# Kernel tuning notes

Measured on AMD Instinct MI355X. Metric: run time of the kernel, lower is better.

The kernel has to match this reference:

```python
import jax, jax.numpy as jnp
import numpy as np

TAU = 2.0        # LIF membrane time constant
VTH = 1.0        # spike threshold
VRESET = 0.0     # hard reset voltage
ALPHA = 2.0      # ATan surrogate alpha
LN_EPS = 1e-5


@jax.custom_vjp
def atan_spike(x):
    # Heaviside forward, ATan surrogate backward (spikingjelly surrogate.ATan)
    return (x >= 0.0).astype(x.dtype)

def _atan_fwd(x):
    return atan_spike(x), x

def _atan_bwd(x, g):
    z = (jnp.pi / 2.0) * ALPHA * x
    return (g * (ALPHA / 2.0) / (1.0 + z * z),)

atan_spike.defvjp(_atan_fwd, _atan_bwd)


def layer_norm(x, w, b):
    mu = jnp.mean(x, axis=-1, keepdims=True)
    var = jnp.mean(jnp.square(x - mu), axis=-1, keepdims=True)
    return (x - mu) * jax.lax.rsqrt(var + LN_EPS) * w + b


def time_shift(x):
    # x: [B,T,C] -> x shifted by one step in time, zero-padded at t=0
    return jnp.pad(x, ((0, 0), (1, 0), (0, 0)))[:, :-1]


def wkv(time_decay, time_first, k, v):
    # Numerically-stable RWKV WKV recurrence. k, v: [B,T,C]
    w = -jnp.exp(time_decay)  # [C]
    u = time_first            # [C]
    B, T, C = k.shape
    kT = jnp.moveaxis(k, 1, 0)  # [T,B,C]
    vT = jnp.moveaxis(v, 1, 0)
    init = (jnp.zeros((B, C), k.dtype),
            jnp.zeros((B, C), k.dtype),
            jnp.full((B, C), -1e38, k.dtype))

    def step(carry, kv_t):
        aa, bb, pp = carry
        kt, vt = kv_t
        ww = u + kt
        p = jnp.maximum(pp, ww)
        e1 = jnp.exp(pp - p)
        e2 = jnp.exp(ww - p)
        y = (e1 * aa + e2 * vt) / (e1 * bb + e2)
        ww2 = pp + w
        p2 = jnp.maximum(ww2, kt)
        e1b = jnp.exp(ww2 - p2)
        e2b = jnp.exp(kt - p2)
        return (e1b * aa + e2b * vt, e1b * bb + e2b, p2), y

    _, yT = jax.lax.scan(step, init, (kT, vT))
    return jnp.moveaxis(yT, 0, 1)  # [B,T,C]


def lif(x):
    # MultiStepLIFNode: tau=2, decay_input=True, v_th=1, hard reset to 0.
    # Recurrence runs over the sequence dim (permute(1,0,2) in torch is layout only).
    xT = jnp.moveaxis(x, 1, 0)  # [T,B,C]
    v0 = jnp.zeros_like(xT[0])

    def step(v, xt):
        v = v + (xt - (v - VRESET)) / TAU
        s = atan_spike(v - VTH)
        v = (1.0 - s) * v + s * VRESET
        return v, s

    _, sT = jax.lax.scan(step, v0, xT)
    return jnp.moveaxis(sT, 0, 1)


def rwkv_time_mix(x, time_decay, time_first, mix_k, mix_v, mix_r, Wk, Wv, Wr, Wo):
    xx = time_shift(x)
    xk = x * mix_k + xx * (1.0 - mix_k)
    xv = x * mix_v + xx * (1.0 - mix_v)
    xr = x * mix_r + xx * (1.0 - mix_r)
    k = jnp.einsum('btc,cd->btd', xk, Wk)
    v = jnp.einsum('btc,cd->btd', xv, Wv)
    r = jax.nn.sigmoid(jnp.einsum('btc,cd->btd', xr, Wr))
    y = wkv(time_decay, time_first, k, v)
    return jnp.einsum('btc,cd->btd', r * y, Wo)


def rwkv_channel_mix(x, mix_k, mix_r, Wk, Wv, Wr):
    xx = time_shift(x)
    xk = x * mix_k + xx * (1.0 - mix_k)
    xr = x * mix_r + xx * (1.0 - mix_r)
    k = jnp.square(jax.nn.relu(jnp.einsum('btc,ch->bth', xk, Wk)))  # relu^2
    kv = jnp.einsum('bth,hc->btc', k, Wv)
    return jax.nn.sigmoid(jnp.einsum('btc,cd->btd', xr, Wr)) * kv


def setup_inputs() -> dict:
    key = jax.random.key(0)
    B, T, C, H = 8, 2048, 768, 3072
    ks = jax.random.split(key, 20)
    p = lambda k, shape, s=0.02: (jax.random.normal(k, shape, jnp.float32) * s)
    u = lambda k, shape: jax.random.uniform(k, shape, jnp.float32)
    return {
        'x': jax.random.normal(ks[0], (B, T, C), jnp.float32),
        'ln1_w': jnp.ones((C,), jnp.float32), 'ln1_b': jnp.zeros((C,), jnp.float32),
        'ln2_w': jnp.ones((C,), jnp.float32), 'ln2_b': jnp.zeros((C,), jnp.float32),
        'att_time_decay': p(ks[1], (C,), 1.0),
        'att_time_first': p(ks[2], (C,), 1.0),
        'att_mix_k': u(ks[3], (C,)), 'att_mix_v': u(ks[4], (C,)), 'att_mix_r': u(ks[5], (C,)),
        'att_Wk': p(ks[6], (C, C)), 'att_Wv': p(ks[7], (C, C)),
        'att_Wr': p(ks[8], (C, C)), 'att_Wo': p(ks[9], (C, C)),
        'ffn_mix_k': u(ks[10], (C,)), 'ffn_mix_r': u(ks[11], (C,)),
        'ffn_Wk': p(ks[12], (C, H)), 'ffn_Wv': p(ks[13], (H, C)), 'ffn_Wr': p(ks[14], (C, C)),
    }


def reference(x, ln1_w, ln1_b, ln2_w, ln2_b,
              att_time_decay, att_time_first, att_mix_k, att_mix_v, att_mix_r,
              att_Wk, att_Wv, att_Wr, att_Wo,
              ffn_mix_k, ffn_mix_r, ffn_Wk, ffn_Wv, ffn_Wr):
    # Block.forward with layer_id != 0 (no ln0, att path); dropout in eval mode.
    a = rwkv_time_mix(layer_norm(x, ln1_w, ln1_b), att_time_decay, att_time_first,
                      att_mix_k, att_mix_v, att_mix_r, att_Wk, att_Wv, att_Wr, att_Wo)
    x = x + lif(a)
    f = rwkv_channel_mix(layer_norm(x, ln2_w, ln2_b), ffn_mix_k, ffn_mix_r,
                         ffn_Wk, ffn_Wv, ffn_Wr)
    x = x + lif(f)
    return x
```

## Files before the change

kernel.cpp:

```cpp
#include <hip/hip_runtime.h>

#define B_ 8
#define T_ 2048
#define C_ 768
#define H_ 3072
#define BT_ (B_ * T_)
#define BC_ (B_ * C_)
#define WSEG 128
#define NWSEG 16
#define LSEG 128
#define NLSEG 16
#define LWARM 96

typedef unsigned short u16;
typedef short bf16x8 __attribute__((ext_vector_type(8)));
typedef float f32x4 __attribute__((ext_vector_type(4)));

__device__ __forceinline__ float b2f(u16 u) {
    union { unsigned i; float f; } w; w.i = ((unsigned)u) << 16; return w.f;
}
__device__ __forceinline__ u16 f2b(float f) {
    union { float f; unsigned i; } w; w.f = f;
    return (u16)((w.i + 0x7fffu + ((w.i >> 16) & 1u)) >> 16);
}

typedef __attribute__((address_space(3))) unsigned int lds_u32;
typedef const __attribute__((address_space(1))) unsigned int glb_u32;
__device__ __forceinline__ void gld_lds16(const void* g, void* l) {
    __builtin_amdgcn_global_load_lds((glb_u32*)g, (lds_u32*)l, 16, 0, 0);
}

template<int NOUT>
__global__ void lnmix(const float* __restrict__ x, const float* __restrict__ w,
                      const float* __restrict__ b,
                      const float* __restrict__ m1, const float* __restrict__ m2,
                      const float* __restrict__ m3,
                      u16* __restrict__ o1, u16* __restrict__ o2, u16* __restrict__ o3) {
    int row = blockIdx.x;
    int t = row % T_;
    const float* xr = x + (size_t)row * C_;
    const float* xp = xr - C_;
    int tid = threadIdx.x;
    float s = 0.f, s2 = 0.f, ps = 0.f, ps2 = 0.f;
    for (int i = tid; i < C_; i += 256) {
        float v = xr[i]; s += v; s2 += v * v;
        if (t > 0) { float u = xp[i]; ps += u; ps2 += u * u; }
    }
    for (int off = 32; off > 0; off >>= 1) {
        s += __shfl_down(s, off);  s2 += __shfl_down(s2, off);
        ps += __shfl_down(ps, off); ps2 += __shfl_down(ps2, off);
    }
    __shared__ float red[4][4];
    int wid = tid >> 6, lane = tid & 63;
    if (lane == 0) { red[wid][0] = s; red[wid][1] = s2; red[wid][2] = ps; red[wid][3] = ps2; }
    __syncthreads();
    if (tid == 0) {
        float a0 = 0, a1 = 0, a2 = 0, a3 = 0;
        for (int i = 0; i < 4; ++i) { a0 += red[i][0]; a1 += red[i][1]; a2 += red[i][2]; a3 += red[i][3]; }
        red[0][0] = a0; red[0][1] = a1; red[0][2] = a2; red[0][3] = a3;
    }
    __syncthreads();
    float mu = red[0][0] * (1.f / C_);
    float rs = rsqrtf(red[0][1] * (1.f / C_) - mu * mu + 1e-5f);
    float pmu = red[0][2] * (1.f / C_);
    float prs = rsqrtf(red[0][3] * (1.f / C_) - pmu * pmu + 1e-5f);
    size_t ob = (size_t)row * C_;
    for (int i = tid; i < C_; i += 256) {
        float wi = w[i], bi = b[i];
        float n = (xr[i] - mu) * rs * wi + bi;
        float np = (t > 0) ? (xp[i] - pmu) * prs * wi + bi : 0.f;
        o1[ob + i] = f2b(fmaf(m1[i], n - np, np));
        o2[ob + i] = f2b(fmaf(m2[i], n - np, np));
        if constexpr (NOUT == 3) o3[ob + i] = f2b(fmaf(m3[i], n - np, np));
    }
}

struct TCJ { const float* s; u16* d; int R, Ncol, nbx, b0; };
struct TC7 { TCJ j[7]; };
__global__ void tcast_all(TC7 jobs) {
    __shared__ float t[32][33];
    int bid = blockIdx.x;
    int ji = 0;
#pragma unroll
    for (int k = 1; k < 7; ++k) if (bid >= jobs.j[k].b0) ji = k;
    TCJ jb = jobs.j[ji];
    int local = bid - jb.b0;
    int bx = local % jb.nbx, by = local / jb.nbx;
    int c0 = bx * 32, r0 = by * 32;
    int col = threadIdx.x & 31, rw = threadIdx.x >> 5;
#pragma unroll
    for (int i = 0; i < 4; ++i) {
        int r = rw + i * 8;
        t[r][col] = jb.s[(size_t)(r0 + r) * jb.Ncol + c0 + col];
    }
    __syncthreads();
#pragma unroll
    for (int i = 0; i < 4; ++i) {
        int r = rw + i * 8;
        jb.d[(size_t)(c0 + r) * jb.R + r0 + col] = f2b(t[col][r]);
    }
}

__device__ __forceinline__ void gemm_core(const u16* __restrict__ A,
                                          const u16* __restrict__ WT,
                                          int K, int m0, int n0,
                                          u16* As, u16* Bs, f32x4 acc[4][8]) {
    const int tid = threadIdx.x;
    const int lane = tid & 63, wid = tid >> 6;
    const int wr = wid >> 1, wc = wid & 1;
    const int r16 = lane & 15, g = lane >> 4;

    const int srow = tid >> 2;
    const int sslot = tid & 3;
    const int sx = (srow >> 1) & 3;
    const u16* gA0 = A + (size_t)(m0 + srow) * K + ((sslot ^ sx) << 3);
    const u16* gA1 = gA0 + (size_t)64 * K;
    const u16* gB0 = WT + (size_t)(n0 + srow) * K + ((sslot ^ sx) << 3);
    const u16* gB1 = gB0 + (size_t)64 * K;
    const u16* gB2 = gB0 + (size_t)128 * K;
    const u16* gB3 = gB0 + (size_t)192 * K;
    u16* lA = As + tid * 8;
    u16* lB = Bs + tid * 8;

    int offA[4], offB[8];
#pragma unroll
    for (int m = 0; m < 4; ++m) {
        int row = wr * 64 + m * 16 + r16;
        offA[m] = row * 32 + (g ^ ((row >> 1) & 3)) * 8;
    }
#pragma unroll
    for (int n = 0; n < 8; ++n) {
        int rob = wc * 128 + n * 16 + r16;
        offB[n] = rob * 32 + (g ^ ((rob >> 1) & 3)) * 8;
    }

    gld_lds16(gA0, lA);        gld_lds16(gA1, lA + 2048);
    gld_lds16(gB0, lB);        gld_lds16(gB1, lB + 2048);
    gld_lds16(gB2, lB + 4096); gld_lds16(gB3, lB + 6144);
    gA0 += 32; gA1 += 32; gB0 += 32; gB1 += 32; gB2 += 32; gB3 += 32;
    __syncthreads();

    const int nk = K >> 5;
    int cur = 0;
    for (int kt = 0; kt < nk; ++kt) {
        const int nxt = cur ^ 1;
        if (kt + 1 < nk) {
            u16* pA = lA + nxt * 4096;
            u16* pB = lB + nxt * 8192;
            gld_lds16(gA0, pA);        gld_lds16(gA1, pA + 2048);
            gld_lds16(gB0, pB);        gld_lds16(gB1, pB + 2048);
            gld_lds16(gB2, pB + 4096); gld_lds16(gB3, pB + 6144);
            gA0 += 32; gA1 += 32; gB0 += 32; gB1 += 32; gB2 += 32; gB3 += 32;
        }
        const u16* Ab = As + cur * 4096;
        const u16* Bb = Bs + cur * 8192;
        bf16x8 af[4], bg[8];
#pragma unroll
        for (int m = 0; m < 4; ++m) af[m] = *(const bf16x8*)(Ab + offA[m]);
#pragma unroll
        for (int n = 0; n < 8; ++n) bg[n] = *(const bf16x8*)(Bb + offB[n]);
#pragma unroll
        for (int m = 0; m < 4; ++m)
#pragma unroll
            for (int n = 0; n < 8; ++n)
                acc[m][n] = __builtin_amdgcn_mfma_f32_16x16x32_bf16(af[m], bg[n], acc[m][n], 0, 0, 0);
        __syncthreads();
        cur = nxt;
    }
}

__device__ __forceinline__ void xcd_remap(int& m0, int& n0) {
    const int gx = gridDim.x;
    const int nwg = gx * gridDim.y;
    const int lin = blockIdx.y * gx + blockIdx.x;
    const int q = nwg >> 3, r = nwg & 7;
    const int xcd = lin & 7, pos = lin >> 3;
    const int nid = (xcd < r ? xcd * (q + 1) : r * (q + 1) + (xcd - r) * q) + pos;
    m0 = (nid / gx) << 7;
    n0 = (nid % gx) << 8;
}

template<int MODE, bool EMUL>
__global__ __launch_bounds__(256, 2)
void gemm2(const u16* __restrict__ A, const u16* __restrict__ WT,
           u16* __restrict__ Cout, const u16* __restrict__ Emul, int N, int K) {
    __shared__ u16 As[8192];
    __shared__ u16 Bs[16384];
    int m0, n0;
    xcd_remap(m0, n0);
    f32x4 acc[4][8];
#pragma unroll
    for (int i = 0; i < 4; ++i)
#pragma unroll
        for (int j = 0; j < 8; ++j)
#pragma unroll
            for (int q = 0; q < 4; ++q) acc[i][j][q] = 0.f;
    gemm_core(A, WT, K, m0, n0, As, Bs, acc);

    const int lane = threadIdx.x & 63, wid = threadIdx.x >> 6;
    const int wr = wid >> 1, wc = wid & 1;
    const int r16 = lane & 15, g = lane >> 4;
#pragma unroll
    for (int m = 0; m < 4; ++m)
#pragma unroll
        for (int n = 0; n < 8; ++n)
#pragma unroll
            for (int j = 0; j < 4; ++j) {
                int row = m0 + wr * 64 + m * 16 + g * 4 + j;
                int col = n0 + wc * 128 + n * 16 + r16;
                float v = acc[m][n][j];
                if constexpr (MODE == 1) v = 1.f / (1.f + expf(-v));
                if constexpr (MODE == 2) { v = fmaxf(v, 0.f); v = v * v; }
                size_t o = (size_t)row * N + col;
                if constexpr (EMUL) v *= b2f(Emul[o]);
                Cout[o] = f2b(v);
            }
}

struct P3 {
    const u16 *A0, *A1, *A2;
    const u16 *W0, *W1, *W2;
    u16 *O0, *O1, *O2;
};
__global__ __launch_bounds__(256, 2)
void proj3(P3 p, int N, int K) {
    __shared__ u16 As[8192];
    __shared__ u16 Bs[16384];
    const int z = blockIdx.z;
    const u16* A = (z == 0) ? p.A0 : (z == 1) ? p.A1 : p.A2;
    const u16* W = (z == 0) ? p.W0 : (z == 1) ? p.W1 : p.W2;
    u16* O = (z == 0) ? p.O0 : (z == 1) ? p.O1 : p.O2;
    int m0, n0;
    xcd_remap(m0, n0);
    f32x4 acc[4][8];
#pragma unroll
    for (int i = 0; i < 4; ++i)
#pragma unroll
        for (int j = 0; j < 8; ++j)
#pragma unroll
            for (int q = 0; q < 4; ++q) acc[i][j][q] = 0.f;
    gemm_core(A, W, K, m0, n0, As, Bs, acc);

    const int lane = threadIdx.x & 63, wid = threadIdx.x >> 6;
    const int wr = wid >> 1, wc = wid & 1;
    const int r16 = lane & 15, g = lane >> 4;
    const bool sig = (z == 2);
#pragma unroll
    for (int m = 0; m < 4; ++m)
#pragma unroll
        for (int n = 0; n < 8; ++n)
#pragma unroll
            for (int j = 0; j < 4; ++j) {
                int row = m0 + wr * 64 + m * 16 + g * 4 + j;
                int col = n0 + wc * 128 + n * 16 + r16;
                float v = acc[m][n][j];
                if (sig) v = 1.f / (1.f + expf(-v));
                O[(size_t)row * N + col] = f2b(v);
            }
}

__global__ void wkv_p1(const float* __restrict__ td, const u16* __restrict__ K,
                       const u16* __restrict__ V, float* __restrict__ st) {
    int bc = blockIdx.x * 256 + threadIdx.x;
    int seg = blockIdx.y;
    int b = bc / C_, c = bc - b * C_;
    float w = -expf(td[c]);
    size_t off = (size_t)b * T_ * C_ + (size_t)seg * WSEG * C_ + c;
    float aa = 0.f, bb = 0.f, pp = -1e38f;
#pragma unroll 4
    for (int i = 0; i < WSEG; ++i) {
        float kt = b2f(K[off + (size_t)i * C_]);
        float vt = b2f(V[off + (size_t)i * C_]);
        float ww2 = pp + w;
        float p2 = fmaxf(ww2, kt);
        float e1 = expf(ww2 - p2);
        float e2 = expf(kt - p2);
        aa = e1 * aa + e2 * vt;
        bb = e1 * bb + e2;
        pp = p2;
    }
    int sidx = seg * 3 * BC_ + bc;
    st[sidx] = aa; st[sidx + BC_] = bb; st[sidx + 2 * BC_] = pp;
}

__global__ void wkv_p2(const float* __restrict__ td, const float* __restrict__ st,
                       float* __restrict__ ini) {
    int bc = blockIdx.x * 256 + threadIdx.x;
    int c = bc % C_;
    float wL = -expf(td[c]) * (float)WSEG;
    float aa = 0.f, bb = 0.f, pp = -1e38f;
    for (int s = 0; s < NWSEG; ++s) {
        int sidx = s * 3 * BC_ + bc;
        ini[sidx] = aa; ini[sidx + BC_] = bb; ini[sidx + 2 * BC_] = pp;
        float la = st[sidx], lb = st[sidx + BC_], lp = st[sidx + 2 * BC_];
        float ppw = pp + wL;
        float p = fmaxf(ppw, lp);
        float e1 = expf(ppw - p), e2 = expf(lp - p);
        aa = e1 * aa + e2 * la;
        bb = e1 * bb + e2 * lb;
        pp = p;
    }
}

__global__ void wkv_p3(const float* __restrict__ td, const float* __restrict__ tf,
                       const u16* __restrict__ K, const u16* __restrict__ V,
                       const u16* __restrict__ R, const float* __restrict__ ini,
                       u16* __restrict__ RY) {
    int bc = blockIdx.x * 256 + threadIdx.x;
    int seg = blockIdx.y;
    int b = bc / C_, c = bc - b * C_;
    float w = -expf(td[c]);
    float u = tf[c];
    int sidx = seg * 3 * BC_ + bc;
    float aa = ini[sidx], bb = ini[sidx + BC_], pp = ini[sidx + 2 * BC_];
    size_t off = (size_t)b * T_ * C_ + (size_t)seg * WSEG * C_ + c;
#pragma unroll 4
    for (int i = 0; i < WSEG; ++i) {
        float kt = b2f(K[off + (size_t)i * C_]);
        float vt = b2f(V[off + (size_t)i * C_]);
        float rr = b2f(R[off + (size_t)i * C_]);
        float ww = u + kt;
        float p = fmaxf(pp, ww);
        float e1 = expf(pp - p);
        float e2 = expf(ww - p);
        RY[off + (size_t)i * C_] = f2b(rr * (e1 * aa + e2 * vt) / (e1 * bb + e2));
        float ww2 = pp + w;
        float p2 = fmaxf(ww2, kt);
        float e1b = expf(ww2 - p2);
        float e2b = expf(kt - p2);
        aa = e1b * aa + e2b * vt;
        bb = e1b * bb + e2b;
        pp = p2;
    }
}

__global__ void lif_add_b(const u16* __restrict__ cur, const float* __restrict__ base,
                          float* __restrict__ out) {
    int bc = blockIdx.x * 256 + threadIdx.x;
    int seg = blockIdx.y;
    int b = bc / C_, c = bc - b * C_;
    size_t rowbase = (size_t)b * T_ * C_ + c;
    int t0 = seg * LSEG;
    int tw = t0 - LWARM; if (tw < 0) tw = 0;
    int nw = t0 - tw;
    float v = 0.f;
    const u16* cp = cur + rowbase + (size_t)tw * C_;
#pragma unroll 8
    for (int i = 0; i < nw; ++i) {
        float xt = b2f(cp[(size_t)i * C_]);
        v += (xt - v) * 0.5f;
        v = (v >= 1.f) ? 0.f : v;
    }
    const u16* c2 = cur + rowbase + (size_t)t0 * C_;
    const float* bp = base + rowbase + (size_t)t0 * C_;
    float* op = out + rowbase + (size_t)t0 * C_;
#pragma unroll 8
    for (int i = 0; i < LSEG; ++i) {
        float xt = b2f(c2[(size_t)i * C_]);
        v += (xt - v) * 0.5f;
        float sp = (v >= 1.f) ? 1.f : 0.f;
        op[(size_t)i * C_] = bp[(size_t)i * C_] + sp;
        v = (sp > 0.f) ? 0.f : v;
    }
}

extern "C" void kernel_launch(void* const* d_in, const int* in_sizes, int n_in,
                              void* d_out, int out_size, void* d_ws, size_t ws_size,
                              hipStream_t stream) {
    const float* x    = (const float*)d_in[0];
    const float* ln1w = (const float*)d_in[1];
    const float* ln1b = (const float*)d_in[2];
    const float* ln2w = (const float*)d_in[3];
    const float* ln2b = (const float*)d_in[4];
    const float* td   = (const float*)d_in[5];
    const float* tf   = (const float*)d_in[6];
    const float* amk  = (const float*)d_in[7];
    const float* amv  = (const float*)d_in[8];
    const float* amr  = (const float*)d_in[9];
    const float* aWk  = (const float*)d_in[10];
    const float* aWv  = (const float*)d_in[11];
    const float* aWr  = (const float*)d_in[12];
    const float* aWo  = (const float*)d_in[13];
    const float* fmk  = (const float*)d_in[14];
    const float* fmr  = (const float*)d_in[15];
    const float* fWk  = (const float*)d_in[16];
    const float* fWv  = (const float*)d_in[17];
    const float* fWr  = (const float*)d_in[18];
    float* out = (float*)d_out;

    const size_t NBC = (size_t)BT_ * C_;
    u16* WkT = (u16*)d_ws;
    u16* WvT = WkT + 589824;
    u16* WrT = WvT + 589824;
    u16* WoT = WrT + 589824;
    u16* FrT = WoT + 589824;
    u16* FkT = FrT + 589824;
    u16* FvT = FkT + 2359296;
    float* st  = (float*)(FvT + 2359296);
    float* ini = st + NWSEG * 3 * BC_;
    u16* S0 = (u16*)(ini + NWSEG * 3 * BC_);
    u16* S1 = S0 + NBC;
    u16* S2 = S1 + NBC;
    u16* S3 = S2 + NBC;
    u16* Hbuf = S3 + NBC;
    size_t fixed_b = (size_t)((char*)Hbuf - (char*)d_ws);

    int NCH = 4;
    if (ws_size >= fixed_b + ((size_t)BT_ * H_ + NBC) * 2) NCH = 1;
    else if (ws_size >= fixed_b + ((size_t)(BT_ / 2) * H_ + NBC / 2) * 2) NCH = 2;
    const int CH = BT_ / NCH;
    u16* Fbuf = Hbuf + (size_t)CH * H_;

    u16* Kb = (u16*)d_out;
    u16* Vb = Kb + NBC;

    {
        TC7 jobs;
        const float* srcs[7] = {aWk, aWv, aWr, aWo, fWr, fWk, fWv};
        u16* dsts[7] = {WkT, WvT, WrT, WoT, FrT, FkT, FvT};
        int Rs[7]    = {768, 768, 768, 768, 768, 768, 3072};
        int Ns[7]    = {768, 768, 768, 768, 768, 3072, 768};
        int b0 = 0;
        for (int k = 0; k < 7; ++k) {
            jobs.j[k].s = srcs[k]; jobs.j[k].d = dsts[k];
            jobs.j[k].R = Rs[k]; jobs.j[k].Ncol = Ns[k];
            jobs.j[k].nbx = Ns[k] / 32; jobs.j[k].b0 = b0;
            b0 += (Ns[k] / 32) * (Rs[k] / 32);
        }
        tcast_all<<<b0, 256, 0, stream>>>(jobs);
    }

    lnmix<3><<<BT_, 256, 0, stream>>>(x, ln1w, ln1b, amk, amv, amr, S0, S1, S2);
    {
        P3 p{S0, S1, S2, WkT, WvT, WrT, Kb, Vb, S3};
        proj3<<<dim3(3, 128, 3), 256, 0, stream>>>(p, C_, C_);
    }
    wkv_p1<<<dim3(BC_ / 256, NWSEG), 256, 0, stream>>>(td, Kb, Vb, st);
    wkv_p2<<<BC_ / 256, 256, 0, stream>>>(td, st, ini);
    wkv_p3<<<dim3(BC_ / 256, NWSEG), 256, 0, stream>>>(td, tf, Kb, Vb, S3, ini, S0);
    gemm2<0, false><<<dim3(3, 128), 256, 0, stream>>>(S0, WoT, S1, nullptr, C_, C_);
    lif_add_b<<<dim3(BC_ / 256, NLSEG), 256, 0, stream>>>(S1, x, out);
    lnmix<2><<<BT_, 256, 0, stream>>>(out, ln2w, ln2b, fmk, fmr, nullptr, S0, S1, nullptr);
    gemm2<1, false><<<dim3(3, 128), 256, 0, stream>>>(S1, FrT, S2, nullptr, C_, C_);
    for (int ch = 0; ch < NCH; ++ch) {
        const u16* xk2c = S0 + (size_t)ch * CH * C_;
        const u16* rrc  = S2 + (size_t)ch * CH * C_;
        gemm2<2, false><<<dim3(12, CH / 128), 256, 0, stream>>>(xk2c, FkT, Hbuf, nullptr, H_, C_);
        gemm2<0, true><<<dim3(3, CH / 128), 256, 0, stream>>>(Hbuf, FvT, Fbuf, rrc, C_, H_);
        lif_add_b<<<dim3((CH / T_) * C_ / 256, NLSEG), 256, 0, stream>>>(
            Fbuf, out + (size_t)ch * CH * C_, out + (size_t)ch * CH * C_);
    }
}
```

Measured before the change: 592.9 us.

## Triple-buffer GEMM LDS pipeline and fuse FFN key and receptance GEMMs

The shared GEMM core moves from double to triple buffering in LDS. It issues loads two k-steps ahead and uses explicit vmcnt waits plus a single barrier per iteration, so global-to-LDS traffic overlaps more with the MFMA work. It also merges the FFN key projection (relu squared) and the receptance projection (sigmoid) into one launch when the FFN is not chunked, so the two run side by side in the same grid. LDS per block grows from 48KB to 72KB, which may limit occupancy to fewer than two blocks per CU.

Result: slower. 617.9 us (+4.2%).

```diff
diff --git a/kernel.cpp b/kernel.cpp
--- a/kernel.cpp
+++ b/kernel.cpp
@@ -134,26 +134,36 @@
         offB[n] = rob * 32 + (g ^ ((rob >> 1) & 3)) * 8;
     }
 
-    gld_lds16(gA0, lA);        gld_lds16(gA1, lA + 2048);
-    gld_lds16(gB0, lB);        gld_lds16(gB1, lB + 2048);
-    gld_lds16(gB2, lB + 4096); gld_lds16(gB3, lB + 6144);
-    gA0 += 32; gA1 += 32; gB0 += 32; gB1 += 32; gB2 += 32; gB3 += 32;
-    __syncthreads();
+#define STAGE6(ao, bo) do { \
+        gld_lds16(gA0, lA + (ao));        gld_lds16(gA1, lA + (ao) + 2048); \
+        gld_lds16(gB0, lB + (bo));        gld_lds16(gB1, lB + (bo) + 2048); \
+        gld_lds16(gB2, lB + (bo) + 4096); gld_lds16(gB3, lB + (bo) + 6144); \
+        gA0 += 32; gA1 += 32; gB0 += 32; gB1 += 32; gB2 += 32; gB3 += 32; } while (0)
 
     const int nk = K >> 5;
-    int cur = 0;
+    STAGE6(0, 0);
+    STAGE6(4096, 8192);
+    int wA = 8192, wB = 16384;
+    int rA = 0, rB = 0;
+
     for (int kt = 0; kt < nk; ++kt) {
-        const int nxt = cur ^ 1;
-        if (kt + 1 < nk) {
-            u16* pA = lA + nxt * 4096;
-            u16* pB = lB + nxt * 8192;
-            gld_lds16(gA0, pA);        gld_lds16(gA1, pA + 2048);
-            gld_lds16(gB0, pB);        gld_lds16(gB1, pB + 2048);
-            gld_lds16(gB2, pB + 4096); gld_lds16(gB3, pB + 6144);
-            gA0 += 32; gA1 += 32; gB0 += 32; gB1 += 32; gB2 += 32; gB3 += 32;
+        if (kt < nk - 1) {
+            asm volatile("s_waitcnt vmcnt(6)" ::: "memory");
+        } else {
+            asm volatile("s_waitcnt vmcnt(0)" ::: "memory");
         }
-        const u16* Ab = As + cur * 4096;
-        const u16* Bb = Bs + cur * 8192;
+        __builtin_amdgcn_sched_barrier(0);
+        __builtin_amdgcn_s_barrier();
+        __builtin_amdgcn_sched_barrier(0);
+        if (kt + 2 < nk) {
+            STAGE6(wA, wB);
+            wA += 4096; if (wA == 12288) wA = 0;
+            wB += 8192; if (wB == 24576) wB = 0;
+        }
+        const u16* Ab = As + rA;
+        const u16* Bb = Bs + rB;
+        rA += 4096; if (rA == 12288) rA = 0;
+        rB += 8192; if (rB == 24576) rB = 0;
         bf16x8 af[4], bg[8];
 #pragma unroll
         for (int m = 0; m < 4; ++m) af[m] = *(const bf16x8*)(Ab + offA[m]);
@@ -164,30 +174,30 @@
 #pragma unroll
             for (int n = 0; n < 8; ++n)
                 acc[m][n] = __builtin_amdgcn_mfma_f32_16x16x32_bf16(af[m], bg[n], acc[m][n], 0, 0, 0);
-        __syncthreads();
-        cur = nxt;
-    }
-}
-
-__device__ __forceinline__ void xcd_remap(int& m0, int& n0) {
+    }
+#undef STAGE6
+}
+
+__device__ __forceinline__ void xcd_remap2(int& bx, int& by) {
     const int gx = gridDim.x;
     const int nwg = gx * gridDim.y;
     const int lin = blockIdx.y * gx + blockIdx.x;
     const int q = nwg >> 3, r = nwg & 7;
     const int xcd = lin & 7, pos = lin >> 3;
     const int nid = (xcd < r ? xcd * (q + 1) : r * (q + 1) + (xcd - r) * q) + pos;
-    m0 = (nid / gx) << 7;
-    n0 = (nid % gx) << 8;
+    bx = nid % gx;
+    by = nid / gx;
 }
 
 template<int MODE, bool EMUL>
 __global__ __launch_bounds__(256, 2)
 void gemm2(const u16* __restrict__ A, const u16* __restrict__ WT,
            u16* __restrict__ Cout, const u16* __restrict__ Emul, int N, int K) {
-    __shared__ u16 As[8192];
-    __shared__ u16 Bs[16384];
-    int m0, n0;
-    xcd_remap(m0, n0);
+    __shared__ u16 As[12288];
+    __shared__ u16 Bs[24576];
+    int bx, by;
+    xcd_remap2(bx, by);
+    const int m0 = by << 7, n0 = bx << 8;
     f32x4 acc[4][8];
 #pragma unroll
     for (int i = 0; i < 4; ++i)
@@ -224,14 +234,15 @@
 };
 __global__ __launch_bounds__(256, 2)
 void proj3(P3 p, int N, int K) {
-    __shared__ u16 As[8192];
-    __shared__ u16 Bs[16384];
+    __shared__ u16 As[12288];
+    __shared__ u16 Bs[24576];
     const int z = blockIdx.z;
     const u16* A = (z == 0) ? p.A0 : (z == 1) ? p.A1 : p.A2;
     const u16* W = (z == 0) ? p.W0 : (z == 1) ? p.W1 : p.W2;
     u16* O = (z == 0) ? p.O0 : (z == 1) ? p.O1 : p.O2;
-    int m0, n0;
-    xcd_remap(m0, n0);
+    int bx, by;
+    xcd_remap2(bx, by);
+    const int m0 = by << 7, n0 = bx << 8;
     f32x4 acc[4][8];
 #pragma unroll
     for (int i = 0; i < 4; ++i)
@@ -255,6 +266,50 @@
                 int col = n0 + wc * 128 + n * 16 + r16;
                 float v = acc[m][n][j];
                 if (sig) v = 1.f / (1.f + expf(-v));
+                O[(size_t)row * N + col] = f2b(v);
+            }
+}
+
+struct J2 {
+    const u16 *A0, *W0; u16 *O0;
+    const u16 *A1, *W1; u16 *O1;
+};
+__global__ __launch_bounds__(256, 2)
+void ffn1rr(J2 p, int K) {
+    __shared__ u16 As[12288];
+    __shared__ u16 Bs[24576];
+    int bx, by;
+    xcd_remap2(bx, by);
+    const bool isF = (bx < 12);
+    const u16* A = isF ? p.A0 : p.A1;
+    const u16* W = isF ? p.W0 : p.W1;
+    u16* O = isF ? p.O0 : p.O1;
+    const int N = isF ? 3072 : 768;
+    const int m0 = by << 7;
+    const int n0 = (isF ? bx : bx - 12) << 8;
+    f32x4 acc[4][8];
+#pragma unroll
+    for (int i = 0; i < 4; ++i)
+#pragma unroll
+        for (int j = 0; j < 8; ++j)
+#pragma unroll
+            for (int q = 0; q < 4; ++q) acc[i][j][q] = 0.f;
+    gemm_core(A, W, K, m0, n0, As, Bs, acc);
+
+    const int lane = threadIdx.x & 63, wid = threadIdx.x >> 6;
+    const int wr = wid >> 1, wc = wid & 1;
+    const int r16 = lane & 15, g = lane >> 4;
+#pragma unroll
+    for (int m = 0; m < 4; ++m)
+#pragma unroll
+        for (int n = 0; n < 8; ++n)
+#pragma unroll
+            for (int j = 0; j < 4; ++j) {
+                int row = m0 + wr * 64 + m * 16 + g * 4 + j;
+                int col = n0 + wc * 128 + n * 16 + r16;
+                float v = acc[m][n][j];
+                if (isF) { v = fmaxf(v, 0.f); v = v * v; }
+                else     { v = 1.f / (1.f + expf(-v)); }
                 O[(size_t)row * N + col] = f2b(v);
             }
 }
@@ -441,13 +496,21 @@
     gemm2<0, false><<<dim3(3, 128), 256, 0, stream>>>(S0, WoT, S1, nullptr, C_, C_);
     lif_add_b<<<dim3(BC_ / 256, NLSEG), 256, 0, stream>>>(S1, x, out);
     lnmix<2><<<BT_, 256, 0, stream>>>(out, ln2w, ln2b, fmk, fmr, nullptr, S0, S1, nullptr);
-    gemm2<1, false><<<dim3(3, 128), 256, 0, stream>>>(S1, FrT, S2, nullptr, C_, C_);
-    for (int ch = 0; ch < NCH; ++ch) {
-        const u16* xk2c = S0 + (size_t)ch * CH * C_;
-        const u16* rrc  = S2 + (size_t)ch * CH * C_;
-        gemm2<2, false><<<dim3(12, CH / 128), 256, 0, stream>>>(xk2c, FkT, Hbuf, nullptr, H_, C_);
-        gemm2<0, true><<<dim3(3, CH / 128), 256, 0, stream>>>(Hbuf, FvT, Fbuf, rrc, C_, H_);
-        lif_add_b<<<dim3((CH / T_) * C_ / 256, NLSEG), 256, 0, stream>>>(
-            Fbuf, out + (size_t)ch * CH * C_, out + (size_t)ch * CH * C_);
-    }
-}
+
+    if (NCH == 1) {
+        J2 p{S0, FkT, Hbuf, S1, FrT, S2};
+        ffn1rr<<<dim3(15, 128), 256, 0, stream>>>(p, C_);
+        gemm2<0, true><<<dim3(3, 128), 256, 0, stream>>>(Hbuf, FvT, Fbuf, S2, C_, H_);
+        lif_add_b<<<dim3(BC_ / 256, NLSEG), 256, 0, stream>>>(Fbuf, out, out);
+    } else {
+        gemm2<1, false><<<dim3(3, 128), 256, 0, stream>>>(S1, FrT, S2, nullptr, C_, C_);
+        for (int ch = 0; ch < NCH; ++ch) {
+            const u16* xk2c = S0 + (size_t)ch * CH * C_;
+            const u16* rrc  = S2 + (size_t)ch * CH * C_;
+            gemm2<2, false><<<dim3(12, CH / 128), 256, 0, stream>>>(xk2c, FkT, Hbuf, nullptr, H_, C_);
+            gemm2<0, true><<<dim3(3, CH / 128), 256, 0, stream>>>(Hbuf, FvT, Fbuf, rrc, C_, H_);
+            lif_add_b<<<dim3((CH / T_) * C_ / 256, NLSEG), 256, 0, stream>>>(
+                Fbuf, out + (size_t)ch * CH * C_, out + (size_t)ch * CH * C_);
+        }
+    }
+}
```
